# Performance work log

Hardware: AMD Instinct MI355X
Metric: run time of the kernel (lower is better)

Reference implementation:

```python
import jax, jax.numpy as jnp
import numpy as np

EPS = 1e-5

def _ln(x, g, b):
    mu = jnp.mean(x, axis=-1, keepdims=True)
    var = jnp.var(x, axis=-1, keepdims=True)
    return (x - mu) * jax.lax.rsqrt(var + EPS) * g + b

def setup_inputs() -> dict:
    key = jax.random.key(0)
    ks = jax.random.split(key, 8)
    B, L, D, H = 2, 2048, 1024, 16
    F = 4096
    s = 0.02
    return {
        "x": jax.random.normal(ks[0], (B, L, D), dtype=jnp.float32),
        "attn_mask": jnp.tril(jnp.ones((L, L), dtype=jnp.float32)),
        # weights stored [in, out] (equivalent to torch Linear weight.T)
        "w_qkuv": jax.random.normal(ks[1], (D, 4 * D), dtype=jnp.float32) * s,
        "w_out": jax.random.normal(ks[2], (D, D), dtype=jnp.float32) * s,
        "w1": jax.random.normal(ks[3], (D, F), dtype=jnp.float32) * s,
        "w2": jax.random.normal(ks[4], (F, D), dtype=jnp.float32) * s,
        "w3": jax.random.normal(ks[5], (D, F), dtype=jnp.float32) * s,
        "ln1_g": jnp.ones((D,), jnp.float32), "ln1_b": jnp.zeros((D,), jnp.float32),
        "ln2_g": jnp.ones((D,), jnp.float32), "ln2_b": jnp.zeros((D,), jnp.float32),
        "na_g": jnp.ones((D // H,), jnp.float32), "na_b": jnp.zeros((D // H,), jnp.float32),
    }

def reference(x, attn_mask, w_qkuv, w_out, w1, w2, w3,
              ln1_g, ln1_b, ln2_g, ln2_b, na_g, na_b):
    B, L, D = x.shape
    H = 16
    d = D // H
    # --- SiLU attention sublayer ---
    xn = _ln(x, ln1_g, ln1_b)
    qkuv = jax.nn.silu(xn @ w_qkuv)                       # [B, L, 4D]
    q, k, v, u = jnp.split(qkuv, 4, axis=-1)
    def heads(t):
        return t.reshape(B, L, H, d).transpose(0, 2, 1, 3)  # [B, H, L, d]
    q, k, v, u = heads(q), heads(k), heads(v), heads(u)
    scores = jnp.einsum('bhqd,bhkd->bhqk', q, k) / jnp.sqrt(jnp.float32(d))
    scores = jax.nn.silu(scores) * attn_mask              # broadcast [L, L] over B, H
    a = jnp.einsum('bhqk,bhkd->bhqd', scores, v)          # [B, H, L, d]
    a = _ln(a, na_g, na_b) * u
    a = a.transpose(0, 2, 1, 3).reshape(B, L, D)
    x = x + a @ w_out
    # --- SwiGLU FFN sublayer ---
    xn2 = _ln(x, ln2_g, ln2_b)
    x = x + (jax.nn.silu(xn2 @ w1) * (xn2 @ w3)) @ w2
    return x
```

## Files before the change

kernel.cpp:

```cpp
#include <hip/hip_runtime.h>
#include <hip/hip_bf16.h>

typedef __hip_bfloat16 bf16;
typedef __attribute__((ext_vector_type(8))) short short8;
typedef __attribute__((ext_vector_type(4))) short bfv4;
typedef __attribute__((ext_vector_type(4))) float f32x4;
typedef __attribute__((ext_vector_type(4))) unsigned short us4;

#define LN_EPS 1e-5f

__device__ __forceinline__ float siluf(float x) { return x / (1.f + __expf(-x)); }
__device__ __forceinline__ unsigned short f2bf_bits(float f) {
    bf16 h = __float2bfloat16(f);
    return *reinterpret_cast<unsigned short*>(&h);
}
__device__ __forceinline__ bf16 f2bf(float f) { return __float2bfloat16(f); }
__device__ __forceinline__ float bf2f(bf16 h) { return __bfloat162float(h); }

__device__ __forceinline__ void load_lds16(const void* g, void* l) {
    __builtin_amdgcn_global_load_lds((const __attribute__((address_space(1))) void*)g,
                                     (__attribute__((address_space(3))) void*)l, 16, 0, 0);
}

__device__ __forceinline__ f32x4 mfma16(bfv4 a, bfv4 b, f32x4 c) {
    return __builtin_amdgcn_mfma_f32_16x16x16bf16_1k(a, b, c, 0, 0, 0);
}

__device__ __forceinline__ void drain_and_sync() {
    asm volatile("s_waitcnt vmcnt(0)" ::: "memory");
    __builtin_amdgcn_sched_barrier(0);
    __syncthreads();
}

template <int N>
__device__ __forceinline__ void wait_vmcnt() {
    asm volatile("s_waitcnt vmcnt(%0)" :: "n"(N) : "memory");
}
__device__ __forceinline__ void hard_barrier() {
    __builtin_amdgcn_sched_barrier(0);
    __builtin_amdgcn_s_barrier();
    __builtin_amdgcn_sched_barrier(0);
}
__device__ __forceinline__ void lgkm_barrier() {
    asm volatile("s_waitcnt lgkmcnt(0)" ::: "memory");
    __builtin_amdgcn_sched_barrier(0);
    __builtin_amdgcn_s_barrier();
    __builtin_amdgcn_sched_barrier(0);
}

__device__ __forceinline__ int xcd_swz(int bid, int nwg) {
    return (bid & 7) * (nwg >> 3) + (bid >> 3);
}

__global__ __launch_bounds__(256) void transpose_cast(
    const float* __restrict__ src, bf16* __restrict__ dst, int K, int N)
{
    __shared__ float t[32][33];
    const int nb = blockIdx.x << 5, kb = blockIdx.y << 5;
    const int tx = threadIdx.x, ty = threadIdx.y;
#pragma unroll
    for (int i = ty; i < 32; i += 8) t[i][tx] = src[(size_t)(kb + i) * N + nb + tx];
    __syncthreads();
#pragma unroll
    for (int i = ty; i < 32; i += 8) dst[(size_t)(nb + i) * K + kb + tx] = f2bf(t[tx][i]);
}

__global__ __launch_bounds__(256) void ln_cast(
    const float* __restrict__ x, const float* __restrict__ g, const float* __restrict__ be,
    bf16* __restrict__ out)
{
    const int row = blockIdx.x, tid = threadIdx.x;
    const float4 v = ((const float4*)(x + (size_t)row * 1024))[tid];
    float s = v.x + v.y + v.z + v.w;
    float ss = v.x * v.x + v.y * v.y + v.z * v.z + v.w * v.w;
#pragma unroll
    for (int o = 32; o; o >>= 1) { s += __shfl_down(s, o); ss += __shfl_down(ss, o); }
    __shared__ float red[10];
    const int wid = tid >> 6, lane = tid & 63;
    if (lane == 0) { red[wid] = s; red[4 + wid] = ss; }
    __syncthreads();
    if (tid == 0) {
        float S = red[0] + red[1] + red[2] + red[3];
        float SS = red[4] + red[5] + red[6] + red[7];
        float mu = S * (1.f / 1024.f);
        red[8] = mu;
        red[9] = rsqrtf(SS * (1.f / 1024.f) - mu * mu + LN_EPS);
    }
    __syncthreads();
    const float mu = red[8], rstd = red[9];
    const float4 gg = ((const float4*)g)[tid];
    const float4 bb = ((const float4*)be)[tid];
    us4 o;
    o[0] = f2bf_bits((v.x - mu) * rstd * gg.x + bb.x);
    o[1] = f2bf_bits((v.y - mu) * rstd * gg.y + bb.y);
    o[2] = f2bf_bits((v.z - mu) * rstd * gg.z + bb.z);
    o[3] = f2bf_bits((v.w - mu) * rstd * gg.w + bb.w);
    ((us4*)(out + (size_t)row * 1024))[tid] = o;
}

template <int EPI>
__global__ __launch_bounds__(512, 2) void gemm8(
    const bf16* __restrict__ A, const bf16* __restrict__ BT,
    bf16* __restrict__ outp, const bf16* __restrict__ mulsrc,
    int M, int N, int K)
{
    __shared__ __align__(16) bf16 lds[2][2][256 * 64];
    const int tid = threadIdx.x;
    const int wid = tid >> 6, lane = tid & 63;
    const int lhi = lane >> 4, llo = lane & 15;
    const int nby = M >> 8;
    const int bid = xcd_swz((int)blockIdx.x, (int)gridDim.x);
    const int by = bid % nby, bx = bid / nby;
    const int row0 = by << 8, col0 = bx << 8;
    const int wr = wid >> 2, wc = wid & 3;
    const int wbase = wid << 6;

    auto stage_tile = [&](const bf16* src, int r0, int k0, char* ldsbase) {
#pragma unroll
        for (int it = 0; it < 4; ++it) {
            const int p = it * 512 + wbase + lane;
            const int r = p >> 3, pc = p & 7;
            const int lc = pc ^ (r & 7);
            load_lds16(src + (size_t)(r0 + r) * K + k0 + lc * 8,
                       ldsbase + (size_t)(it * 512 + wbase) * 16);
        }
    };
    auto stageA = [&](int t) { stage_tile(A, row0, t << 6, (char*)lds[t & 1][0]); };
    auto stageB = [&](int t) { stage_tile(BT, col0, t << 6, (char*)lds[t & 1][1]); };

    f32x4 acc[8][4] = {};

    stageA(0); stageB(0); stageA(1); stageB(1);
    wait_vmcnt<8>();
    hard_barrier();

    const int KT = K >> 6;
    for (int t = 0; t < KT; ++t) {
        const int buf = t & 1;
        const char* lAc = (const char*)lds[buf][0];
        const char* lBc = (const char*)lds[buf][1];

        short8 af[4], b0[2], b1[2];
        auto ldA = [&](int mh, int kk) {
#pragma unroll
            for (int m = 0; m < 4; ++m) {
                const int ra = wr * 128 + mh * 64 + m * 16 + llo;
                af[m] = *(const short8*)(lAc + ra * 128 + (((kk * 4 + lhi) ^ (ra & 7)) << 4));
            }
        };
        auto ldB = [&](short8* bf_, int nh, int kk) {
#pragma unroll
            for (int n = 0; n < 2; ++n) {
                const int rb = wc * 64 + nh * 32 + n * 16 + llo;
                bf_[n] = *(const short8*)(lBc + rb * 128 + (((kk * 4 + lhi) ^ (rb & 7)) << 4));
            }
        };
        auto mfma_q = [&](int mh, int nh, short8* bf_) {
            __builtin_amdgcn_s_setprio(1);
#pragma unroll
            for (int m = 0; m < 4; ++m)
#pragma unroll
                for (int n = 0; n < 2; ++n)
                    acc[mh * 4 + m][nh * 2 + n] =
                        __builtin_amdgcn_mfma_f32_16x16x32_bf16(af[m], bf_[n], acc[mh * 4 + m][nh * 2 + n], 0, 0, 0);
            __builtin_amdgcn_s_setprio(0);
        };

#pragma unroll
        for (int kk = 0; kk < 2; ++kk) {
            ldA(0, kk); ldB(b0, 0, kk);
            mfma_q(0, 0, b0);
            ldB(b1, 1, kk);
            mfma_q(0, 1, b1);
            ldA(1, kk);
            mfma_q(1, 0, b0);
            mfma_q(1, 1, b1);
        }

        lgkm_barrier();
        if (t + 2 < KT) {
            stageA(t + 2); stageB(t + 2);
            wait_vmcnt<8>();
            hard_barrier();
        } else if (t + 1 < KT) {
            wait_vmcnt<0>();
            hard_barrier();
        }
    }

#pragma unroll
    for (int m = 0; m < 8; ++m) {
        const int rbase = row0 + wr * 128 + m * 16 + lhi * 4;
#pragma unroll
        for (int n = 0; n < 4; ++n) {
            const int c = col0 + wc * 64 + n * 16 + llo;
#pragma unroll
            for (int r = 0; r < 4; ++r) {
                const size_t idx = (size_t)(rbase + r) * N + c;
                const float v = acc[m][n][r];
                if constexpr (EPI == 0) outp[idx] = f2bf(siluf(v));
                else                    outp[idx] = f2bf(v * bf2f(mulsrc[idx]));
            }
        }
    }
}

__global__ __launch_bounds__(512, 2) void gemm_w13_8(
    const bf16* __restrict__ A, const bf16* __restrict__ B1T, const bf16* __restrict__ B3T,
    bf16* __restrict__ outp, int M, int N, int K)
{
    __shared__ __align__(16) bf16 lA[2][256 * 64];
    __shared__ __align__(16) bf16 lB1[2][128 * 64];
    __shared__ __align__(16) bf16 lB3[2][128 * 64];
    const int tid = threadIdx.x;
    const int wid = tid >> 6, lane = tid & 63;
    const int lhi = lane >> 4, llo = lane & 15;
    const int nby = M >> 8;
    const int bid = xcd_swz((int)blockIdx.x, (int)gridDim.x);
    const int by = bid % nby, bx = bid / nby;
    const int row0 = by << 8, col0 = bx << 7;
    const int wr = wid >> 2, wc = wid & 3;
    const int wbase = wid << 6;

    auto stage_rows = [&](const bf16* src, int r0, int k0, char* ldsbase, int nit) {
        for (int it = 0; it < nit; ++it) {
            const int p = it * 512 + wbase + lane;
            const int r = p >> 3, pc = p & 7;
            const int lc = pc ^ (r & 7);
            load_lds16(src + (size_t)(r0 + r) * K + k0 + lc * 8,
                       ldsbase + (size_t)(it * 512 + wbase) * 16);
        }
    };
    auto stageT = [&](int t) {
        const int k0 = t << 6, buf = t & 1;
        stage_rows(A, row0, k0, (char*)lA[buf], 4);
        stage_rows(B1T, col0, k0, (char*)lB1[buf], 2);
        stage_rows(B3T, col0, k0, (char*)lB3[buf], 2);
    };

    f32x4 acc1[8][2] = {}, acc3[8][2] = {};

    stageT(0); stageT(1);
    wait_vmcnt<8>();
    hard_barrier();

    const int KT = K >> 6;
    for (int t = 0; t < KT; ++t) {
        const int buf = t & 1;
        const char* lAc = (const char*)lA[buf];
        const char* lB1c = (const char*)lB1[buf];
        const char* lB3c = (const char*)lB3[buf];

        short8 af[4], b1[2], b3[2];
        auto ldA = [&](int mh, int kk) {
#pragma unroll
            for (int m = 0; m < 4; ++m) {
                const int ra = wr * 128 + mh * 64 + m * 16 + llo;
                af[m] = *(const short8*)(lAc + ra * 128 + (((kk * 4 + lhi) ^ (ra & 7)) << 4));
            }
        };
        auto ldB = [&](int kk) {
#pragma unroll
            for (int n = 0; n < 2; ++n) {
                const int rb = wc * 32 + n * 16 + llo;
                const int so = (((kk * 4 + lhi) ^ (rb & 7)) << 4);
                b1[n] = *(const short8*)(lB1c + rb * 128 + so);
                b3[n] = *(const short8*)(lB3c + rb * 128 + so);
            }
        };
        auto mfma_h = [&](int mh) {
            __builtin_amdgcn_s_setprio(1);
#pragma unroll
            for (int m = 0; m < 4; ++m)
#pragma unroll
                for (int n = 0; n < 2; ++n) {
                    acc1[mh * 4 + m][n] = __builtin_amdgcn_mfma_f32_16x16x32_bf16(af[m], b1[n], acc1[mh * 4 + m][n], 0, 0, 0);
                    acc3[mh * 4 + m][n] = __builtin_amdgcn_mfma_f32_16x16x32_bf16(af[m], b3[n], acc3[mh * 4 + m][n], 0, 0, 0);
                }
            __builtin_amdgcn_s_setprio(0);
        };

#pragma unroll
        for (int kk = 0; kk < 2; ++kk) {
            ldB(kk);
            ldA(0, kk);
            mfma_h(0);
            ldA(1, kk);
            mfma_h(1);
        }

        lgkm_barrier();
        if (t + 2 < KT) {
            stageT(t + 2);
            wait_vmcnt<8>();
            hard_barrier();
        } else if (t + 1 < KT) {
            wait_vmcnt<0>();
            hard_barrier();
        }
    }

#pragma unroll
    for (int m = 0; m < 8; ++m) {
        const int rbase = row0 + wr * 128 + m * 16 + lhi * 4;
#pragma unroll
        for (int n = 0; n < 2; ++n) {
            const int c = col0 + wc * 32 + n * 16 + llo;
#pragma unroll
            for (int r = 0; r < 4; ++r) {
                const size_t idx = (size_t)(rbase + r) * N + c;
                outp[idx] = f2bf(siluf(acc1[m][n][r]) * acc3[m][n][r]);
            }
        }
    }
}

__global__ __launch_bounds__(256) void gemm_btc(
    const bf16* __restrict__ A, const bf16* __restrict__ BT,
    float* __restrict__ outp, const float* __restrict__ resid,
    int M, int N, int K)
{
    __shared__ __align__(16) bf16 lA[2][128 * 64];
    __shared__ __align__(16) bf16 lB[2][64 * 64];
    const int tid = threadIdx.x;
    const int wid = tid >> 6, lane = tid & 63;
    const int lhi = lane >> 4, llo = lane & 15;
    const int nby = M >> 7;
    const int bid = xcd_swz((int)blockIdx.x, (int)gridDim.x);
    const int by = bid % nby, bx = bid / nby;
    const int row0 = by << 7, col0 = bx << 6;
    const int wr = wid >> 1, wc = wid & 1;
    const int wbase = wid << 6;

    auto stage_tile = [&](const bf16* src, int r0, int k0, char* ldsbase, int nit) {
        for (int it = 0; it < nit; ++it) {
            const int p = it * 256 + wbase + lane;
            const int r = p >> 3, pc = p & 7;
            const int lc = pc ^ (r & 7);
            load_lds16(src + (size_t)(r0 + r) * K + k0 + lc * 8,
                       ldsbase + (size_t)(it * 256 + wbase) * 16);
        }
    };
    auto stageT = [&](int t) {
        stage_tile(A, row0, t << 6, (char*)lA[t & 1], 4);
        stage_tile(BT, col0, t << 6, (char*)lB[t & 1], 2);
    };

    f32x4 acc[4][2] = {};

    stageT(0); stageT(1);
    wait_vmcnt<6>();
    hard_barrier();

    const int KT = K >> 6;
    for (int t = 0; t < KT; ++t) {
        const int buf = t & 1;
        const char* lAc = (const char*)lA[buf];
        const char* lBc = (const char*)lB[buf];

        short8 af[4], bfr[2];
        auto ldA = [&](int kk) {
#pragma unroll
            for (int m = 0; m < 4; ++m) {
                const int ra = wr * 64 + m * 16 + llo;
                af[m] = *(const short8*)(lAc + ra * 128 + (((kk * 4 + lhi) ^ (ra & 7)) << 4));
            }
        };
        auto ldB = [&](int kk) {
#pragma unroll
            for (int n = 0; n < 2; ++n) {
                const int rb = wc * 32 + n * 16 + llo;
                bfr[n] = *(const short8*)(lBc + rb * 128 + (((kk * 4 + lhi) ^ (rb & 7)) << 4));
            }
        };

#pragma unroll
        for (int kk = 0; kk < 2; ++kk) {
            ldA(kk); ldB(kk);
            __builtin_amdgcn_s_setprio(1);
#pragma unroll
            for (int m = 0; m < 4; ++m)
#pragma unroll
                for (int n = 0; n < 2; ++n)
                    acc[m][n] = __builtin_amdgcn_mfma_f32_16x16x32_bf16(af[m], bfr[n], acc[m][n], 0, 0, 0);
            __builtin_amdgcn_s_setprio(0);
        }

        lgkm_barrier();
        if (t + 2 < KT) {
            stageT(t + 2);
            wait_vmcnt<6>();
            hard_barrier();
        } else if (t + 1 < KT) {
            wait_vmcnt<0>();
            hard_barrier();
        }
    }

#pragma unroll
    for (int m = 0; m < 4; ++m) {
        const int rbase = row0 + wr * 64 + m * 16 + lhi * 4;
#pragma unroll
        for (int n = 0; n < 2; ++n) {
            const int c = col0 + wc * 32 + n * 16 + llo;
#pragma unroll
            for (int r = 0; r < 4; ++r) {
                const size_t idx = (size_t)(rbase + r) * N + c;
                outp[idx] = resid[idx] + acc[m][n][r];
            }
        }
    }
}

__global__ __launch_bounds__(256) void v_trans(const bf16* __restrict__ qkuv, bf16* __restrict__ v_t)
{
    __shared__ bf16 t[64][65];
    const int bh = blockIdx.y;
    const int b = bh >> 4, h = bh & 15;
    const int l0 = blockIdx.x << 6;
    const int tx = threadIdx.x, ty = threadIdx.y;
#pragma unroll
    for (int i = ty; i < 64; i += 4)
        t[i][tx] = qkuv[(size_t)(b * 2048 + l0 + i) * 4096 + 2048 + h * 64 + tx];
    __syncthreads();
#pragma unroll
    for (int i = ty; i < 64; i += 4)
        v_t[(size_t)(bh * 64 + i) * 2048 + l0 + tx] = t[tx][i];
}

__global__ __launch_bounds__(512) void attn_kernel(
    const bf16* __restrict__ qkuv, const bf16* __restrict__ v_t,
    const float* __restrict__ nag, const float* __restrict__ nab,
    bf16* __restrict__ au)
{
    __shared__ __align__(16) bf16 lK[2][128 * 64];
    __shared__ __align__(16) bf16 lV[2][64 * 128];
    const int tid = threadIdx.x;
    const int wid = tid >> 6, lane = tid & 63;
    const int lhi = lane >> 4, llo = lane & 15;
    const int vb = xcd_swz((int)blockIdx.x, (int)gridDim.x);
    const int bh = vb >> 4;
    const int qt = 15 - (vb & 15);
    const int b = bh >> 4, h = bh & 15;
    const int q0 = qt << 7;
    const bf16* Qb = qkuv + (size_t)b * 2048 * 4096 + h * 64;
    const bf16* Kb = Qb + 1024;
    const bf16* Ub = Qb + 3072;
    const bf16* Vb = v_t + (size_t)bh * 64 * 2048;
    const int wbase = wid << 6;

    auto stage = [&](int kt_s, int buf) {
        const int koff = kt_s << 7;
        char* lKc = (char*)lK[buf];
        char* lVc = (char*)lV[buf];
#pragma unroll
        for (int it = 0; it < 2; ++it) {
            const int p = it * 512 + wbase + lane;
            const int r = p >> 3, pc = p & 7;
            const int lc = pc ^ (r & 7);
            load_lds16(Kb + (size_t)(koff + r) * 4096 + lc * 8, lKc + (it * 512 + wbase) * 16);
        }
#pragma unroll
        for (int it = 0; it < 2; ++it) {
            const int p = it * 512 + wbase + lane;
            const int d = p >> 4, pc = p & 15;
            const int lc = pc ^ (d & 15);
            load_lds16(Vb + (size_t)d * 2048 + koff + lc * 8, lVc + (it * 512 + wbase) * 16);
        }
    };

    short8 qb[2];
#pragma unroll
    for (int kk = 0; kk < 2; ++kk)
        qb[kk] = *(const short8*)(Qb + (size_t)(q0 + wid * 16 + llo) * 4096 + kk * 32 + lhi * 8);

    f32x4 acc2[4] = {};

    stage(0, 0);

    for (int kt = 0; kt <= qt; ++kt) {
        const int cur = kt & 1;
        drain_and_sync();
        if (kt < qt) stage(kt + 1, cur ^ 1);
        const char* lKc = (const char*)lK[cur];
        const char* lVc = (const char*)lV[cur];

        const bool diag = (kt == qt);
#pragma unroll
        for (int m = 0; m < 8; ++m) {
            if (diag && m > wid) break;
            const int rK = m * 16 + llo;
            const int sw = rK & 7;
            short8 ak0 = *(const short8*)(lKc + rK * 128 + ((lhi ^ sw) << 4));
            short8 ak1 = *(const short8*)(lKc + rK * 128 + (((4 + lhi) ^ sw) << 4));
            f32x4 s = {};
            s = __builtin_amdgcn_mfma_f32_16x16x32_bf16(ak0, qb[0], s, 0, 0, 0);
            s = __builtin_amdgcn_mfma_f32_16x16x32_bf16(ak1, qb[1], s, 0, 0, 0);
            const bool mask = diag && (m == wid);
            bfv4 a16;
#pragma unroll
            for (int r = 0; r < 4; ++r) {
                float xx = s[r] * 0.125f;
                xx = xx * __builtin_amdgcn_rcpf(1.f + __expf(-xx));
                if (mask && (lhi * 4 + r > llo)) xx = 0.f;
                a16[r] = (short)f2bf_bits(xx);
            }
#pragma unroll
            for (int dcol = 0; dcol < 4; ++dcol) {
                const int d = dcol * 16 + llo;
                const int lcV = m * 2 + (lhi >> 1);
                bfv4 bv = *(const bfv4*)(lVc + d * 256 + ((lcV ^ llo) << 4) + (lhi & 1) * 8);
                acc2[dcol] = mfma16(a16, bv, acc2[dcol]);
            }
        }
    }

#pragma unroll
    for (int r = 0; r < 4; ++r) {
        float vv[4];
        float s = 0.f, ss = 0.f;
#pragma unroll
        for (int dc = 0; dc < 4; ++dc) { vv[dc] = acc2[dc][r]; s += vv[dc]; ss += vv[dc] * vv[dc]; }
#pragma unroll
        for (int o = 1; o < 16; o <<= 1) { s += __shfl_xor(s, o); ss += __shfl_xor(ss, o); }
        const float mu = s * (1.f / 64.f);
        const float rstd = rsqrtf(ss * (1.f / 64.f) - mu * mu + LN_EPS);
        const int q = wid * 16 + lhi * 4 + r;
        const size_t grow = q0 + q;
#pragma unroll
        for (int dc = 0; dc < 4; ++dc) {
            const int c = dc * 16 + llo;
            const float nv = (vv[dc] - mu) * rstd * nag[c] + nab[c];
            const float uu = bf2f(Ub[grow * 4096 + c]);
            au[(size_t)(b * 2048 + grow) * 1024 + h * 64 + c] = f2bf(nv * uu);
        }
    }
}

extern "C" void kernel_launch(void* const* d_in, const int* in_sizes, int n_in,
                              void* d_out, int out_size, void* d_ws, size_t ws_size,
                              hipStream_t stream)
{
    const float* x      = (const float*)d_in[0];
    const float* w_qkuv = (const float*)d_in[2];
    const float* w_out  = (const float*)d_in[3];
    const float* w1     = (const float*)d_in[4];
    const float* w2     = (const float*)d_in[5];
    const float* w3     = (const float*)d_in[6];
    const float* ln1g   = (const float*)d_in[7];
    const float* ln1b   = (const float*)d_in[8];
    const float* ln2g   = (const float*)d_in[9];
    const float* ln2b   = (const float*)d_in[10];
    const float* nag    = (const float*)d_in[11];
    const float* nab    = (const float*)d_in[12];
    float* out = (float*)d_out;

    char* ws = (char*)d_ws;
    size_t off = 0;
    auto alloc = [&](size_t bytes) { void* p = ws + off; off += (bytes + 255) & ~(size_t)255; return p; };
    const size_t M = 4096;
    bf16* wqkuvT = (bf16*)alloc(4096ull * 1024 * 2);
    bf16* woutT  = (bf16*)alloc(1024ull * 1024 * 2);
    bf16* w1T    = (bf16*)alloc(4096ull * 1024 * 2);
    bf16* w3T    = (bf16*)alloc(4096ull * 1024 * 2);
    bf16* w2T    = (bf16*)alloc(1024ull * 4096 * 2);
    bf16* xn     = (bf16*)alloc(M * 1024 * 2);
    bf16* qkuv   = (bf16*)alloc(M * 4096 * 2);
    bf16* vt     = (bf16*)alloc(32ull * 64 * 2048 * 2);
    bf16* aub    = (bf16*)alloc(M * 1024 * 2);
    float* x2    = (float*)alloc(M * 1024 * 4);
    bf16* xn2    = (bf16*)alloc(M * 1024 * 2);
    bf16* h1     = (bf16*)alloc(M * 4096 * 2);
    (void)ws_size; (void)in_sizes; (void)n_in; (void)out_size;

    dim3 tb(32, 8);
    transpose_cast<<<dim3(4096 / 32, 1024 / 32), tb, 0, stream>>>(w_qkuv, wqkuvT, 1024, 4096);
    transpose_cast<<<dim3(1024 / 32, 1024 / 32), tb, 0, stream>>>(w_out, woutT, 1024, 1024);
    transpose_cast<<<dim3(4096 / 32, 1024 / 32), tb, 0, stream>>>(w1, w1T, 1024, 4096);
    transpose_cast<<<dim3(4096 / 32, 1024 / 32), tb, 0, stream>>>(w3, w3T, 1024, 4096);
    transpose_cast<<<dim3(1024 / 32, 4096 / 32), tb, 0, stream>>>(w2, w2T, 4096, 1024);

    ln_cast<<<M, 256, 0, stream>>>(x, ln1g, ln1b, xn);

    gemm8<0><<<dim3((M / 256) * (4096 / 256)), 512, 0, stream>>>(xn, wqkuvT, qkuv, nullptr, M, 4096, 1024);

    v_trans<<<dim3(2048 / 64, 32), dim3(64, 4), 0, stream>>>(qkuv, vt);

    attn_kernel<<<dim3(512), 512, 0, stream>>>(qkuv, vt, nag, nab, aub);

    gemm_btc<<<dim3((M / 128) * (1024 / 64)), 256, 0, stream>>>(aub, woutT, x2, x, M, 1024, 1024);

    ln_cast<<<M, 256, 0, stream>>>(x2, ln2g, ln2b, xn2);

    gemm_w13_8<<<dim3((M / 256) * (4096 / 128)), 512, 0, stream>>>(xn2, w1T, w3T, h1, M, 4096, 1024);

    gemm_btc<<<dim3((M / 128) * (1024 / 64)), 256, 0, stream>>>(h1, w2T, out, x2, M, 1024, 4096);
}
```

Before: 310.5 us.

## Restructure GEMM main loops into barrier-separated ping-pong phases with interleaved staging

Rewrites the K-loop of two bf16 GEMM kernels so each tile is processed in four barrier-delimited phases. Each phase loads LDS fragments, issues the next tile's global-to-LDS copy, then runs an MFMA block at raised priority between workgroup barriers. The prefetch distance drops from two tiles to one, so next-tile loads overlap the current tile's MFMAs instead of being issued after them. The extra barriers per tile add synchronisation overhead and may stall waves if the phases are unbalanced.

```diff
diff --git a/kernel.cpp b/kernel.cpp
--- a/kernel.cpp
+++ b/kernel.cpp
@@ -43,6 +43,20 @@
 }
 __device__ __forceinline__ void lgkm_barrier() {
     asm volatile("s_waitcnt lgkmcnt(0)" ::: "memory");
+    __builtin_amdgcn_sched_barrier(0);
+    __builtin_amdgcn_s_barrier();
+    __builtin_amdgcn_sched_barrier(0);
+}
+
+__device__ __forceinline__ void phase_pre() {
+    __builtin_amdgcn_sched_barrier(0);
+    __builtin_amdgcn_s_barrier();
+    asm volatile("s_waitcnt lgkmcnt(0)" ::: "memory");
+    __builtin_amdgcn_sched_barrier(0);
+    __builtin_amdgcn_s_setprio(1);
+}
+__device__ __forceinline__ void phase_post() {
+    __builtin_amdgcn_s_setprio(0);
     __builtin_amdgcn_sched_barrier(0);
     __builtin_amdgcn_s_barrier();
     __builtin_amdgcn_sched_barrier(0);
@@ -130,62 +144,57 @@
 
     f32x4 acc[8][4] = {};
 
-    stageA(0); stageB(0); stageA(1); stageB(1);
-    wait_vmcnt<8>();
+    stageA(0); stageB(0);
+    wait_vmcnt<0>();
     hard_barrier();
 
     const int KT = K >> 6;
     for (int t = 0; t < KT; ++t) {
-        const int buf = t & 1;
-        const char* lAc = (const char*)lds[buf][0];
-        const char* lBc = (const char*)lds[buf][1];
-
-        short8 af[4], b0[2], b1[2];
-        auto ldA = [&](int mh, int kk) {
-#pragma unroll
-            for (int m = 0; m < 4; ++m) {
-                const int ra = wr * 128 + mh * 64 + m * 16 + llo;
-                af[m] = *(const short8*)(lAc + ra * 128 + (((kk * 4 + lhi) ^ (ra & 7)) << 4));
-            }
-        };
-        auto ldB = [&](short8* bf_, int nh, int kk) {
-#pragma unroll
-            for (int n = 0; n < 2; ++n) {
-                const int rb = wc * 64 + nh * 32 + n * 16 + llo;
-                bf_[n] = *(const short8*)(lBc + rb * 128 + (((kk * 4 + lhi) ^ (rb & 7)) << 4));
-            }
-        };
-        auto mfma_q = [&](int mh, int nh, short8* bf_) {
-            __builtin_amdgcn_s_setprio(1);
-#pragma unroll
-            for (int m = 0; m < 4; ++m)
-#pragma unroll
-                for (int n = 0; n < 2; ++n)
-                    acc[mh * 4 + m][nh * 2 + n] =
-                        __builtin_amdgcn_mfma_f32_16x16x32_bf16(af[m], bf_[n], acc[mh * 4 + m][nh * 2 + n], 0, 0, 0);
-            __builtin_amdgcn_s_setprio(0);
-        };
-
-#pragma unroll
-        for (int kk = 0; kk < 2; ++kk) {
-            ldA(0, kk); ldB(b0, 0, kk);
-            mfma_q(0, 0, b0);
-            ldB(b1, 1, kk);
-            mfma_q(0, 1, b1);
-            ldA(1, kk);
-            mfma_q(1, 0, b0);
-            mfma_q(1, 1, b1);
-        }
-
-        lgkm_barrier();
-        if (t + 2 < KT) {
-            stageA(t + 2); stageB(t + 2);
-            wait_vmcnt<8>();
-            hard_barrier();
-        } else if (t + 1 < KT) {
-            wait_vmcnt<0>();
-            hard_barrier();
-        }
+        const bool more = (t + 1 < KT);
+        const char* lAc = (const char*)lds[t & 1][0];
+        const char* lBc = (const char*)lds[t & 1][1];
+
+        short8 a0[2][4], a1[2][4], b0[2][2], b1[2][2];
+        auto ldA = [&](short8 af[2][4], int mh) {
+#pragma unroll
+            for (int kk = 0; kk < 2; ++kk)
+#pragma unroll
+                for (int m = 0; m < 4; ++m) {
+                    const int ra = wr * 128 + mh * 64 + m * 16 + llo;
+                    af[kk][m] = *(const short8*)(lAc + ra * 128 + (((kk * 4 + lhi) ^ (ra & 7)) << 4));
+                }
+        };
+        auto ldB = [&](short8 bf_[2][2], int nh) {
+#pragma unroll
+            for (int kk = 0; kk < 2; ++kk)
+#pragma unroll
+                for (int n = 0; n < 2; ++n) {
+                    const int rb = wc * 64 + nh * 32 + n * 16 + llo;
+                    bf_[kk][n] = *(const short8*)(lBc + rb * 128 + (((kk * 4 + lhi) ^ (rb & 7)) << 4));
+                }
+        };
+        auto mfma_q = [&](int mh, int nh, short8 af[2][4], short8 bf_[2][2]) {
+#pragma unroll
+            for (int kk = 0; kk < 2; ++kk)
+#pragma unroll
+                for (int m = 0; m < 4; ++m)
+#pragma unroll
+                    for (int n = 0; n < 2; ++n)
+                        acc[mh * 4 + m][nh * 2 + n] =
+                            __builtin_amdgcn_mfma_f32_16x16x32_bf16(af[kk][m], bf_[kk][n], acc[mh * 4 + m][nh * 2 + n], 0, 0, 0);
+        };
+
+        ldA(a0, 0); ldB(b0, 0);
+        if (more) stageA(t + 1);
+        phase_pre(); mfma_q(0, 0, a0, b0); phase_post();
+        ldB(b1, 1);
+        if (more) stageB(t + 1);
+        phase_pre(); mfma_q(0, 1, a0, b1); phase_post();
+        ldA(a1, 1);
+        phase_pre(); mfma_q(1, 1, a1, b1); phase_post();
+        phase_pre(); mfma_q(1, 0, a1, b0); phase_post();
+
+        if (more) { wait_vmcnt<0>(); hard_barrier(); }
     }
 
 #pragma unroll
@@ -231,73 +240,65 @@
                        ldsbase + (size_t)(it * 512 + wbase) * 16);
         }
     };
-    auto stageT = [&](int t) {
-        const int k0 = t << 6, buf = t & 1;
-        stage_rows(A, row0, k0, (char*)lA[buf], 4);
-        stage_rows(B1T, col0, k0, (char*)lB1[buf], 2);
-        stage_rows(B3T, col0, k0, (char*)lB3[buf], 2);
+    auto stageA = [&](int t) { stage_rows(A, row0, t << 6, (char*)lA[t & 1], 4); };
+    auto stageB = [&](int t) {
+        stage_rows(B1T, col0, t << 6, (char*)lB1[t & 1], 2);
+        stage_rows(B3T, col0, t << 6, (char*)lB3[t & 1], 2);
     };
 
     f32x4 acc1[8][2] = {}, acc3[8][2] = {};
 
-    stageT(0); stageT(1);
-    wait_vmcnt<8>();
+    stageA(0); stageB(0);
+    wait_vmcnt<0>();
     hard_barrier();
 
     const int KT = K >> 6;
     for (int t = 0; t < KT; ++t) {
-        const int buf = t & 1;
-        const char* lAc = (const char*)lA[buf];
-        const char* lB1c = (const char*)lB1[buf];
-        const char* lB3c = (const char*)lB3[buf];
-
-        short8 af[4], b1[2], b3[2];
-        auto ldA = [&](int mh, int kk) {
+        const bool more = (t + 1 < KT);
+        const char* lAc = (const char*)lA[t & 1];
+        const char* lB1c = (const char*)lB1[t & 1];
+        const char* lB3c = (const char*)lB3[t & 1];
+
+        short8 b1f[2], b3f[2];
+        auto ldA4 = [&](short8 af[4], int mh, int kk) {
 #pragma unroll
             for (int m = 0; m < 4; ++m) {
                 const int ra = wr * 128 + mh * 64 + m * 16 + llo;
                 af[m] = *(const short8*)(lAc + ra * 128 + (((kk * 4 + lhi) ^ (ra & 7)) << 4));
             }
         };
-        auto ldB = [&](int kk) {
+        auto ldBk = [&](int kk) {
 #pragma unroll
             for (int n = 0; n < 2; ++n) {
                 const int rb = wc * 32 + n * 16 + llo;
                 const int so = (((kk * 4 + lhi) ^ (rb & 7)) << 4);
-                b1[n] = *(const short8*)(lB1c + rb * 128 + so);
-                b3[n] = *(const short8*)(lB3c + rb * 128 + so);
-            }
-        };
-        auto mfma_h = [&](int mh) {
-            __builtin_amdgcn_s_setprio(1);
+                b1f[n] = *(const short8*)(lB1c + rb * 128 + so);
+                b3f[n] = *(const short8*)(lB3c + rb * 128 + so);
+            }
+        };
+        auto mfma_p = [&](short8 af[4], int mh) {
 #pragma unroll
             for (int m = 0; m < 4; ++m)
 #pragma unroll
                 for (int n = 0; n < 2; ++n) {
-                    acc1[mh * 4 + m][n] = __builtin_amdgcn_mfma_f32_16x16x32_bf16(af[m], b1[n], acc1[mh * 4 + m][n], 0, 0, 0);
-                    acc3[mh * 4 + m][n] = __builtin_amdgcn_mfma_f32_16x16x32_bf16(af[m], b3[n], acc3[mh * 4 + m][n], 0, 0, 0);
+                    acc1[mh * 4 + m][n] = __builtin_amdgcn_mfma_f32_16x16x32_bf16(af[m], b1f[n], acc1[mh * 4 + m][n], 0, 0, 0);
+                    acc3[mh * 4 + m][n] = __builtin_amdgcn_mfma_f32_16x16x32_bf16(af[m], b3f[n], acc3[mh * 4 + m][n], 0, 0, 0);
                 }
-            __builtin_amdgcn_s_setprio(0);
-        };
-
-#pragma unroll
-        for (int kk = 0; kk < 2; ++kk) {
-            ldB(kk);
-            ldA(0, kk);
-            mfma_h(0);
-            ldA(1, kk);
-            mfma_h(1);
-        }
-
-        lgkm_barrier();
-        if (t + 2 < KT) {
-            stageT(t + 2);
-            wait_vmcnt<8>();
-            hard_barrier();
-        } else if (t + 1 < KT) {
-            wait_vmcnt<0>();
-            hard_barrier();
-        }
+        };
+
+        short8 af[4];
+        ldA4(af, 0, 0); ldBk(0);
+        if (more) stageA(t + 1);
+        phase_pre(); mfma_p(af, 0); phase_post();
+        ldA4(af, 1, 0);
+        if (more) stageB(t + 1);
+        phase_pre(); mfma_p(af, 1); phase_post();
+        ldA4(af, 0, 1); ldBk(1);
+        phase_pre(); mfma_p(af, 0); phase_post();
+        ldA4(af, 1, 1);
+        phase_pre(); mfma_p(af, 1); phase_post();
+
+        if (more) { wait_vmcnt<0>(); hard_barrier(); }
     }
 
 #pragma unroll
```

Result: no change. 306.1 us (-1.4%).
